# Performance work log

Measured on AMD Instinct MI355X. Metric: run time of the kernel, lower is better.

Reference implementation:

```python
import jax, jax.numpy as jnp
import numpy as np

B, N, D = 8, 1024, 768
H, Z = 12, 64          # num_heads, head_dim (D = H*Z)
HID = 3072             # int(D * mlp_ratio)


def setup_inputs() -> dict:
    key = jax.random.key(0)
    k1, k2, k3, k4 = jax.random.split(key, 4)
    s = 0.02
    x = jax.random.normal(k1, (B, N, D), dtype=jnp.float32)
    Wq = jax.random.normal(k2, (D, D), dtype=jnp.float32) * s
    Wk = jax.random.normal(k3, (D, D), dtype=jnp.float32) * s
    betas = jnp.full((H,), Z ** -0.5, dtype=jnp.float32)
    W_mlp = jax.random.normal(k4, (HID, D), dtype=jnp.float32) * s
    return {"x": x, "Wq": Wq, "Wk": Wk, "betas": betas, "W_mlp": W_mlp}


def reference(x, Wq, Wk, betas, W_mlp):
    # --- KQ-aligned attention ---
    # torch Linear: y = x @ W.T ; weight shape [out=D, in=D]
    Q = jnp.einsum('bnd,ed->bne', x, Wq).reshape(B, N, H, Z).transpose(0, 2, 1, 3)  # bhqz
    K = jnp.einsum('bnd,ed->bne', x, Wk).reshape(B, N, H, Z).transpose(0, 2, 1, 3)  # bhkz
    Wq_r = Wq.reshape(H, Z, D)
    Wk_r = Wk.reshape(H, Z, D)
    F1 = jnp.einsum('hzd,bhkz->bkhd', Wq_r, K)
    F2 = jnp.einsum('hzd,bhqz->bqhd', Wk_r, Q)
    scores = jnp.einsum('bhqz,bhkz,h->bhqk', Q, K, betas)
    attn = jax.nn.softmax(scores, axis=-1)
    T1 = jnp.einsum('bkhd,bhqk->bqd', F1, attn)
    T2 = jnp.einsum('bqhd,bhqk->bkd', F2, attn)
    # --- symmetric-weight Hopfield MLP (bias=False) ---
    hid = jax.nn.relu(jnp.einsum('bnd,hd->bnh', x, W_mlp))
    mlp = jnp.einsum('bnh,hd->bnd', hid, W_mlp)
    return T1 + T2 + mlp
```

## Files before the change

### kernel.cpp

```cpp
#include <hip/hip_runtime.h>
#include <hip/hip_bf16.h>

#define Bq 8
#define Nq 1024
#define Dq 768
#define Hq 12
#define Zq 64
#define HIDq 3072
#define BN (Bq*Nq)
#define QKP 1536

typedef unsigned short u16;
typedef short s16x8 __attribute__((ext_vector_type(8)));
typedef float f32x4 __attribute__((ext_vector_type(4)));
typedef unsigned short u16x4 __attribute__((ext_vector_type(4)));

#define MFMA16 __builtin_amdgcn_mfma_f32_16x16x32_bf16
#define GLOAD16(g, l) __builtin_amdgcn_global_load_lds( \
    (const __attribute__((address_space(1))) void*)(const void*)(g), \
    (__attribute__((address_space(3))) void*)(l), 16, 0, 0)

__device__ __forceinline__ u16 f2bf(float f) {
  unsigned u = __float_as_uint(f);
  return (u16)((u + 0x7FFFu + ((u >> 16) & 1u)) >> 16);
}

__device__ __forceinline__ void xcd_swizzle(int gx, int gy, int& bx, int& by) {
  int l = blockIdx.y * gx + blockIdx.x;
  int c = l & 7, j = l >> 3;
  by = c * (gy >> 3) + j / gx;
  bx = j % gx;
}

__global__ __launch_bounds__(256) void cvt_bf16(const float* __restrict__ in,
                                                u16* __restrict__ out, int n) {
  int i = (blockIdx.x * 256 + threadIdx.x) * 4;
  if (i >= n) return;
  float4 v = *(const float4*)&in[i];
  u16x4 o; o[0] = f2bf(v.x); o[1] = f2bf(v.y); o[2] = f2bf(v.z); o[3] = f2bf(v.w);
  *(u16x4*)&out[i] = o;
}

__global__ __launch_bounds__(256) void cvt_tr(const float* __restrict__ in,
                                              u16* __restrict__ out, u16* __restrict__ outT,
                                              int C, int out_p, int outT_p) {
  __shared__ u16 T[64][72];
  const int t = threadIdx.x;
  const int r0 = blockIdx.y * 64, c0 = blockIdx.x * 64;
  const int r = t >> 3, c8 = (t & 7) * 8;
#pragma unroll
  for (int p = 0; p < 2; p++) {
    const float* ip = &in[(size_t)(r0 + r + p * 32) * C + c0 + c8];
    float4 v0 = *(const float4*)ip, v1 = *(const float4*)(ip + 4);
    u16 tmp[8] = {f2bf(v0.x), f2bf(v0.y), f2bf(v0.z), f2bf(v0.w),
                  f2bf(v1.x), f2bf(v1.y), f2bf(v1.z), f2bf(v1.w)};
    *(uint4*)&out[(size_t)(r0 + r + p * 32) * out_p + c0 + c8] = *(uint4*)tmp;
    *(uint4*)&T[r + p * 32][c8] = *(uint4*)tmp;
  }
  __syncthreads();
#pragma unroll
  for (int p = 0; p < 2; p++) {
    int oc = r + p * 32;
    u16 tmp[8];
#pragma unroll
    for (int j = 0; j < 8; j++) tmp[j] = T[c8 + j][oc];
    *(uint4*)&outT[(size_t)(c0 + oc) * outT_p + r0 + c8] = *(uint4*)tmp;
  }
}

__global__ __launch_bounds__(256) void transpose_bf16(
    const u16* __restrict__ in, u16* __restrict__ out,
    int in_pitch, int out_pitch, int inner_n,
    long in_bs_o, long in_bs_i, long out_bs_o, long out_bs_i) {
  __shared__ u16 T[64][72];
  const int t = threadIdx.x;
  const int bz = blockIdx.z;
  const long iboff = (long)(bz / inner_n) * in_bs_o + (long)(bz % inner_n) * in_bs_i;
  const long oboff = (long)(bz / inner_n) * out_bs_o + (long)(bz % inner_n) * out_bs_i;
  const u16* ip = in + iboff + (long)(blockIdx.y * 64) * in_pitch + blockIdx.x * 64;
  u16* op = out + oboff + (long)(blockIdx.x * 64) * out_pitch + blockIdx.y * 64;
  const int r = t >> 3, c8 = (t & 7) * 8;
#pragma unroll
  for (int p = 0; p < 2; p++)
    *(uint4*)&T[r + p * 32][c8] = *(const uint4*)(ip + (size_t)(r + p * 32) * in_pitch + c8);
  __syncthreads();
#pragma unroll
  for (int p = 0; p < 2; p++) {
    int oc = r + p * 32;
    u16 tmp[8];
#pragma unroll
    for (int j = 0; j < 8; j++) tmp[j] = T[c8 + j][oc];
    *(uint4*)(op + (size_t)oc * out_pitch + c8) = *(uint4*)tmp;
  }
}

template<bool RELU>
__global__ __launch_bounds__(256) void gemm_bf16(
    const u16* __restrict__ A, const u16* __restrict__ B, u16* __restrict__ C,
    int M, int N, int K) {
  __shared__ u16 As[2][128 * 32];
  __shared__ u16 Bs[2][128 * 32];
  int bx, by;
  xcd_swizzle(gridDim.x, gridDim.y, bx, by);
  const int t = threadIdx.x, l = t & 63, w = t >> 6;
  const int lq = l & 15, quad = l >> 4;
  const int bm = by * 128, bn = bx * 128;
  const int wm = (w & 1) * 64, wn = (w >> 1) * 64;
  f32x4 acc[4][4];
#pragma unroll
  for (int i = 0; i < 4; i++)
#pragma unroll
    for (int j = 0; j < 4; j++) acc[i][j] = (f32x4){0.f, 0.f, 0.f, 0.f};

  auto stage = [&](int k0, int bufi) {
#pragma unroll
    for (int p = 0; p < 2; p++) {
      int idx = p * 256 + t;
      GLOAD16(A + (size_t)(bm + (idx >> 2)) * K + k0 + (idx & 3) * 8, &As[bufi][idx * 8]);
      GLOAD16(B + (size_t)(bn + (idx >> 2)) * K + k0 + (idx & 3) * 8, &Bs[bufi][idx * 8]);
    }
  };
  stage(0, 0);
  const int nIter = K >> 5;
  for (int it = 0; it < nIter; it++) {
    __syncthreads();
    if (it + 1 < nIter) stage((it + 1) * 32, (it + 1) & 1);
    const int bi = it & 1;
    s16x8 af[4], bf[4];
#pragma unroll
    for (int mt = 0; mt < 4; mt++)
      af[mt] = *(const s16x8*)&As[bi][(wm + mt * 16 + lq) * 32 + quad * 8];
#pragma unroll
    for (int nt = 0; nt < 4; nt++)
      bf[nt] = *(const s16x8*)&Bs[bi][(wn + nt * 16 + lq) * 32 + quad * 8];
#pragma unroll
    for (int mt = 0; mt < 4; mt++)
#pragma unroll
      for (int nt = 0; nt < 4; nt++)
        acc[mt][nt] = MFMA16(af[mt], bf[nt], acc[mt][nt], 0, 0, 0);
  }
#pragma unroll
  for (int mt = 0; mt < 4; mt++)
#pragma unroll
    for (int nt = 0; nt < 4; nt++) {
      int row = bm + wm + mt * 16 + quad * 4;
      int col = bn + wn + nt * 16 + lq;
#pragma unroll
      for (int r = 0; r < 4; r++) {
        float v = acc[mt][nt][r];
        if (RELU) v = fmaxf(v, 0.f);
        C[(size_t)(row + r) * N + col] = f2bf(v);
      }
    }
}

__global__ __launch_bounds__(256) void gemm_out2(
    const u16* __restrict__ AV12, const u16* __restrict__ hid,
    const u16* __restrict__ WqkT, const u16* __restrict__ WmT,
    float* __restrict__ out) {
  __shared__ u16 As[2][128 * 64];
  __shared__ u16 Bs[2][64 * 64];
  int bx, by;
  xcd_swizzle(gridDim.x, gridDim.y, bx, by);
  const int t = threadIdx.x, l = t & 63, w = t >> 6;
  const int lq = l & 15, quad = l >> 4;
  const int bm = by * 128, bn = bx * 64;
  const int wm = w * 32;
  f32x4 acc[2][4];
#pragma unroll
  for (int i = 0; i < 2; i++)
#pragma unroll
    for (int j = 0; j < 4; j++) acc[i][j] = (f32x4){0.f, 0.f, 0.f, 0.f};

  auto stage = [&](int tl, int bufi) {
    const u16* A; const u16* B; int pitch, k0;
    if (tl < 24) { A = AV12; B = WqkT; pitch = QKP;  k0 = tl * 64; }
    else         { A = hid;  B = WmT;  pitch = HIDq; k0 = (tl - 24) * 64; }
#pragma unroll
    for (int p = 0; p < 4; p++) {
      int idx = p * 256 + t, ks = idx >> 9, rem = idx & 511;
      GLOAD16(A + (size_t)(bm + (rem >> 2)) * pitch + k0 + ks * 32 + (rem & 3) * 8,
              &As[bufi][idx * 8]);
    }
#pragma unroll
    for (int p = 0; p < 2; p++) {
      int idx = p * 256 + t, ks = idx >> 8, rem = idx & 255;
      GLOAD16(B + (size_t)(bn + (rem >> 2)) * pitch + k0 + ks * 32 + (rem & 3) * 8,
              &Bs[bufi][idx * 8]);
    }
  };
  stage(0, 0);
  for (int tl = 0; tl < 72; tl++) {
    __syncthreads();
    if (tl + 1 < 72) stage(tl + 1, (tl + 1) & 1);
    const int bi = tl & 1;
#pragma unroll
    for (int ks = 0; ks < 2; ks++) {
      s16x8 af[2], bf[4];
#pragma unroll
      for (int mt = 0; mt < 2; mt++)
        af[mt] = *(const s16x8*)&As[bi][ks * 4096 + (wm + mt * 16 + lq) * 32 + quad * 8];
#pragma unroll
      for (int nt = 0; nt < 4; nt++)
        bf[nt] = *(const s16x8*)&Bs[bi][ks * 2048 + (nt * 16 + lq) * 32 + quad * 8];
#pragma unroll
      for (int mt = 0; mt < 2; mt++)
#pragma unroll
        for (int nt = 0; nt < 4; nt++)
          acc[mt][nt] = MFMA16(af[mt], bf[nt], acc[mt][nt], 0, 0, 0);
    }
  }
#pragma unroll
  for (int mt = 0; mt < 2; mt++)
#pragma unroll
    for (int nt = 0; nt < 4; nt++) {
      int row = bm + wm + mt * 16 + quad * 4;
      int col = bn + nt * 16 + lq;
#pragma unroll
      for (int r = 0; r < 4; r++)
        out[(size_t)(row + r) * Dq + col] = acc[mt][nt][r];
    }
}

__global__ __launch_bounds__(256) void attn_pass1(
    const u16* __restrict__ QKb, const u16* __restrict__ KbT,
    const float* __restrict__ betas, u16* __restrict__ AV12,
    float* __restrict__ lg) {
  __shared__ u16 Qs[2][64][32];
  __shared__ u16 Ks[2][64][32];
  __shared__ u16 Kts[2][64][32];
  __shared__ u16 Ps[64][72];
  __shared__ float red[4][64];
  __shared__ float li[64];

  const int t = threadIdx.x, l = t & 63, w = t >> 6;
  const int lq = l & 15, quad = l >> 4;
  const int c = blockIdx.x & 7, j = blockIdx.x >> 3;
  const int bh = c * 12 + j / 16, qt = j % 16;
  const int b = bh / Hq, h = bh % Hq;
  const int q0 = qt * 64;
  const float beta = betas[h];
  const u16* Qh = QKb + (size_t)(b * Nq) * QKP + h * 64;
  const u16* Kh = Qh + Dq;
  const u16* KTh = KbT + (size_t)bh * 64 * Nq;
  u16* QsF = &Qs[0][0][0]; u16* KsF = &Ks[0][0][0]; u16* KtsF = &Kts[0][0][0];

#pragma unroll
  for (int p = 0; p < 2; p++) {
    int idx = p * 256 + t;
    GLOAD16(Qh + (size_t)(q0 + ((idx >> 2) & 63)) * QKP + (idx >> 8) * 32 + (idx & 3) * 8,
            QsF + idx * 8);
  }
  __syncthreads();
  s16x8 bqf[2][4];
#pragma unroll
  for (int zs = 0; zs < 2; zs++)
#pragma unroll
    for (int nt = 0; nt < 4; nt++)
      bqf[zs][nt] = *(const s16x8*)&Qs[zs][nt * 16 + lq][quad * 8];

  float lsum[4] = {0.f, 0.f, 0.f, 0.f};
  f32x4 ao[4];
#pragma unroll
  for (int nt = 0; nt < 4; nt++) ao[nt] = (f32x4){0.f, 0.f, 0.f, 0.f};

  for (int kt = 0; kt < 16; kt++) {
#pragma unroll
    for (int p = 0; p < 2; p++) {
      int idx = p * 256 + t;
      GLOAD16(Kh + (size_t)(kt * 64 + ((idx >> 2) & 63)) * QKP + (idx >> 8) * 32 + (idx & 3) * 8,
              KsF + idx * 8);
      GLOAD16(KTh + (size_t)((idx >> 2) & 63) * Nq + kt * 64 + (idx >> 8) * 32 + (idx & 3) * 8,
              KtsF + idx * 8);
    }
    __syncthreads();
    f32x4 sc[4];
#pragma unroll
    for (int nt = 0; nt < 4; nt++) sc[nt] = (f32x4){0.f, 0.f, 0.f, 0.f};
#pragma unroll
    for (int zs = 0; zs < 2; zs++) {
      s16x8 a = *(const s16x8*)&Ks[zs][w * 16 + lq][quad * 8];
#pragma unroll
      for (int nt = 0; nt < 4; nt++)
        sc[nt] = MFMA16(a, bqf[zs][nt], sc[nt], 0, 0, 0);
    }
#pragma unroll
    for (int nt = 0; nt < 4; nt++) {
      u16x4 pk;
#pragma unroll
      for (int r = 0; r < 4; r++) {
        float e = __expf(sc[nt][r] * beta);
        lsum[nt] += e;
        pk[r] = f2bf(e);
      }
      *(u16x4*)&Ps[nt * 16 + lq][w * 16 + quad * 4] = pk;
    }
    __syncthreads();
#pragma unroll
    for (int ks = 0; ks < 2; ks++) {
      s16x8 a = *(const s16x8*)&Ps[w * 16 + lq][ks * 32 + quad * 8];
#pragma unroll
      for (int nt = 0; nt < 4; nt++) {
        s16x8 bk = *(const s16x8*)&Kts[ks][nt * 16 + lq][quad * 8];
        ao[nt] = MFMA16(a, bk, ao[nt], 0, 0, 0);
      }
    }
    __syncthreads();
  }
#pragma unroll
  for (int nt = 0; nt < 4; nt++) {
    float v = lsum[nt];
    v += __shfl_xor(v, 16, 64);
    v += __shfl_xor(v, 32, 64);
    if (l < 16) red[w][nt * 16 + lq] = v;
  }
  __syncthreads();
  if (t < 64) {
    float s = red[0][t] + red[1][t] + red[2][t] + red[3][t];
    lg[(size_t)bh * Nq + q0 + t] = s;
    li[t] = 1.0f / s;
  }
  __syncthreads();
  u16* Oh = AV12 + (size_t)(b * Nq + q0) * QKP + h * 64;
  float lr[4];
#pragma unroll
  for (int r = 0; r < 4; r++) lr[r] = li[w * 16 + quad * 4 + r];
#pragma unroll
  for (int nt = 0; nt < 4; nt++)
#pragma unroll
    for (int r = 0; r < 4; r++)
      Oh[(size_t)(w * 16 + quad * 4 + r) * QKP + nt * 16 + lq] = f2bf(ao[nt][r] * lr[r]);
}

__global__ __launch_bounds__(256) void attn_pass2(
    const u16* __restrict__ QKb, const u16* __restrict__ QbT,
    const float* __restrict__ betas, u16* __restrict__ AV12,
    const float* __restrict__ lg) {
  __shared__ u16 Qs[2][64][32];
  __shared__ u16 Qts[2][64][32];
  __shared__ u16 Ks[2][64][32];
  __shared__ u16 Pts[64][72];
  __shared__ float li_s[64];

  const int t = threadIdx.x, l = t & 63, w = t >> 6;
  const int lq = l & 15, quad = l >> 4;
  const int c = blockIdx.x & 7, j = blockIdx.x >> 3;
  const int bh = c * 12 + j / 16, kt = j % 16;
  const int b = bh / Hq, h = bh % Hq;
  const int k0 = kt * 64;
  const float beta = betas[h];
  const u16* Qh = QKb + (size_t)(b * Nq) * QKP + h * 64;
  const u16* Kh = Qh + Dq;
  const u16* QTh = QbT + (size_t)bh * 64 * Nq;
  u16* QsF = &Qs[0][0][0]; u16* QtsF = &Qts[0][0][0]; u16* KsF = &Ks[0][0][0];

#pragma unroll
  for (int p = 0; p < 2; p++) {
    int idx = p * 256 + t;
    GLOAD16(Kh + (size_t)(k0 + ((idx >> 2) & 63)) * QKP + (idx >> 8) * 32 + (idx & 3) * 8,
            KsF + idx * 8);
  }
  __syncthreads();
  s16x8 bkf[2][4];
#pragma unroll
  for (int zs = 0; zs < 2; zs++)
#pragma unroll
    for (int nt = 0; nt < 4; nt++)
      bkf[zs][nt] = *(const s16x8*)&Ks[zs][nt * 16 + lq][quad * 8];

  f32x4 ao[4];
#pragma unroll
  for (int nt = 0; nt < 4; nt++) ao[nt] = (f32x4){0.f, 0.f, 0.f, 0.f};

  for (int qt = 0; qt < 16; qt++) {
#pragma unroll
    for (int p = 0; p < 2; p++) {
      int idx = p * 256 + t;
      GLOAD16(Qh + (size_t)(qt * 64 + ((idx >> 2) & 63)) * QKP + (idx >> 8) * 32 + (idx & 3) * 8,
              QsF + idx * 8);
      GLOAD16(QTh + (size_t)((idx >> 2) & 63) * Nq + qt * 64 + (idx >> 8) * 32 + (idx & 3) * 8,
              QtsF + idx * 8);
    }
    if (t < 64) li_s[t] = 1.0f / lg[(size_t)bh * Nq + qt * 64 + t];
    __syncthreads();
    f32x4 sc[4];
#pragma unroll
    for (int nt = 0; nt < 4; nt++) sc[nt] = (f32x4){0.f, 0.f, 0.f, 0.f};
#pragma unroll
    for (int zs = 0; zs < 2; zs++) {
      s16x8 a = *(const s16x8*)&Qs[zs][w * 16 + lq][quad * 8];
#pragma unroll
      for (int nt = 0; nt < 4; nt++)
        sc[nt] = MFMA16(a, bkf[zs][nt], sc[nt], 0, 0, 0);
    }
    float lr[4];
#pragma unroll
    for (int r = 0; r < 4; r++) lr[r] = li_s[w * 16 + quad * 4 + r];
#pragma unroll
    for (int nt = 0; nt < 4; nt++) {
      u16x4 pk;
#pragma unroll
      for (int r = 0; r < 4; r++)
        pk[r] = f2bf(__expf(sc[nt][r] * beta) * lr[r]);
      *(u16x4*)&Pts[nt * 16 + lq][w * 16 + quad * 4] = pk;
    }
    __syncthreads();
#pragma unroll
    for (int qs = 0; qs < 2; qs++) {
      s16x8 a = *(const s16x8*)&Pts[w * 16 + lq][qs * 32 + quad * 8];
#pragma unroll
      for (int nt = 0; nt < 4; nt++) {
        s16x8 bq = *(const s16x8*)&Qts[qs][nt * 16 + lq][quad * 8];
        ao[nt] = MFMA16(a, bq, ao[nt], 0, 0, 0);
      }
    }
    __syncthreads();
  }
  u16* Oh = AV12 + (size_t)(b * Nq + k0) * QKP + Dq + h * 64;
#pragma unroll
  for (int nt = 0; nt < 4; nt++)
#pragma unroll
    for (int r = 0; r < 4; r++)
      Oh[(size_t)(w * 16 + quad * 4 + r) * QKP + nt * 16 + lq] = f2bf(ao[nt][r]);
}

extern "C" void kernel_launch(void* const* d_in, const int* in_sizes, int n_in,
                              void* d_out, int out_size, void* d_ws, size_t ws_size,
                              hipStream_t stream) {
  const float* x     = (const float*)d_in[0];
  const float* Wq    = (const float*)d_in[1];
  const float* Wk    = (const float*)d_in[2];
  const float* betas = (const float*)d_in[3];
  const float* Wm    = (const float*)d_in[4];
  float* out = (float*)d_out;

  u16* xb   = (u16*)d_ws;
  u16* Wqkb = xb + (size_t)BN * Dq;
  u16* Wmb  = Wqkb + (size_t)QKP * Dq;
  u16* WqkT = Wmb + (size_t)HIDq * Dq;
  u16* QKb  = WqkT + (size_t)Dq * QKP;
  u16* QbT  = QKb + (size_t)BN * QKP;
  u16* KbT  = QbT + (size_t)Bq * Hq * Zq * Nq;
  u16* AV12 = KbT + (size_t)Bq * Hq * Zq * Nq;
  float* lg = (float*)(AV12 + (size_t)BN * QKP);
  u16* hidb = QKb;
  u16* WmT  = xb;

  dim3 blk(256);
  cvt_bf16<<<(BN * Dq) / 1024, blk, 0, stream>>>(x, xb, BN * Dq);
  cvt_tr<<<dim3(12, 12), blk, 0, stream>>>(Wq, Wqkb, WqkT, Dq, Dq, QKP);
  cvt_tr<<<dim3(12, 12), blk, 0, stream>>>(Wk, Wqkb + (size_t)Dq * Dq, WqkT + Dq, Dq, Dq, QKP);
  cvt_bf16<<<(HIDq * Dq) / 1024, blk, 0, stream>>>(Wm, Wmb, HIDq * Dq);

  gemm_bf16<false><<<dim3(QKP / 128, BN / 128), blk, 0, stream>>>(
      xb, Wqkb, QKb, BN, QKP, Dq);

  transpose_bf16<<<dim3(1, 16, 96), blk, 0, stream>>>(QKb, QbT, QKP, Nq, Hq,
      (long)Nq * QKP, 64, (long)Hq * 64 * Nq, (long)64 * Nq);
  transpose_bf16<<<dim3(1, 16, 96), blk, 0, stream>>>(QKb + Dq, KbT, QKP, Nq, Hq,
      (long)Nq * QKP, 64, (long)Hq * 64 * Nq, (long)64 * Nq);

  attn_pass1<<<Bq * Hq * 16, blk, 0, stream>>>(QKb, KbT, betas, AV12, lg);
  attn_pass2<<<Bq * Hq * 16, blk, 0, stream>>>(QKb, QbT, betas, AV12, lg);

  gemm_bf16<true><<<dim3(HIDq / 128, BN / 128), blk, 0, stream>>>(
      xb, Wmb, hidb, BN, HIDq, Dq);

  transpose_bf16<<<dim3(12, 48, 1), blk, 0, stream>>>(Wmb, WmT, Dq, HIDq, 1, 0, 0, 0, 0);

  gemm_out2<<<dim3(Dq / 64, BN / 128), blk, 0, stream>>>(AV12, hidb, WqkT, WmT, out);
}
```

Before: 363.8 us.

## Split-K final output GEMM across three z-slices with atomic accumulation

The final output GEMM (attention AV12×WqkT plus hidden×WmT, K=4608) is split along K into three 1536-wide slices, one per grid z-index. Each block now computes a larger 128×128 tile with a 32-wide k-step, and partial results are combined with float atomic adds into an output that is zeroed by a memset first. The aim is to put more blocks in flight (the original grid had only 768 blocks each running a long 72-step K loop) and to reuse each staged tile across more MFMAs. The cost is atomic traffic on the fp32 output, an extra memset pass, and a summation order that is no longer deterministic.

```diff
diff --git a/kernel.cpp b/kernel.cpp
--- a/kernel.cpp
+++ b/kernel.cpp
@@ -158,67 +158,62 @@
     const u16* __restrict__ AV12, const u16* __restrict__ hid,
     const u16* __restrict__ WqkT, const u16* __restrict__ WmT,
     float* __restrict__ out) {
-  __shared__ u16 As[2][128 * 64];
-  __shared__ u16 Bs[2][64 * 64];
+  __shared__ u16 As[2][128 * 32];
+  __shared__ u16 Bs[2][128 * 32];
   int bx, by;
   xcd_swizzle(gridDim.x, gridDim.y, bx, by);
+  const int z = blockIdx.z;
   const int t = threadIdx.x, l = t & 63, w = t >> 6;
   const int lq = l & 15, quad = l >> 4;
-  const int bm = by * 128, bn = bx * 64;
-  const int wm = w * 32;
-  f32x4 acc[2][4];
-#pragma unroll
-  for (int i = 0; i < 2; i++)
+  const int bm = by * 128, bn = bx * 128;
+  const int wm = (w & 1) * 64, wn = (w >> 1) * 64;
+
+  const u16* A; const u16* B; int pitch, kbase;
+  if (z == 0) { A = AV12; B = WqkT; pitch = QKP;  kbase = 0; }
+  else        { A = hid;  B = WmT;  pitch = HIDq; kbase = (z - 1) * 1536; }
+
+  f32x4 acc[4][4];
+#pragma unroll
+  for (int i = 0; i < 4; i++)
 #pragma unroll
     for (int j = 0; j < 4; j++) acc[i][j] = (f32x4){0.f, 0.f, 0.f, 0.f};
 
   auto stage = [&](int tl, int bufi) {
-    const u16* A; const u16* B; int pitch, k0;
-    if (tl < 24) { A = AV12; B = WqkT; pitch = QKP;  k0 = tl * 64; }
-    else         { A = hid;  B = WmT;  pitch = HIDq; k0 = (tl - 24) * 64; }
-#pragma unroll
-    for (int p = 0; p < 4; p++) {
-      int idx = p * 256 + t, ks = idx >> 9, rem = idx & 511;
-      GLOAD16(A + (size_t)(bm + (rem >> 2)) * pitch + k0 + ks * 32 + (rem & 3) * 8,
-              &As[bufi][idx * 8]);
-    }
+    const int k0 = kbase + tl * 32;
 #pragma unroll
     for (int p = 0; p < 2; p++) {
-      int idx = p * 256 + t, ks = idx >> 8, rem = idx & 255;
-      GLOAD16(B + (size_t)(bn + (rem >> 2)) * pitch + k0 + ks * 32 + (rem & 3) * 8,
-              &Bs[bufi][idx * 8]);
+      int idx = p * 256 + t;
+      GLOAD16(A + (size_t)(bm + (idx >> 2)) * pitch + k0 + (idx & 3) * 8, &As[bufi][idx * 8]);
+      GLOAD16(B + (size_t)(bn + (idx >> 2)) * pitch + k0 + (idx & 3) * 8, &Bs[bufi][idx * 8]);
     }
   };
   stage(0, 0);
-  for (int tl = 0; tl < 72; tl++) {
-    __syncthreads();
-    if (tl + 1 < 72) stage(tl + 1, (tl + 1) & 1);
+  for (int tl = 0; tl < 48; tl++) {
+    __syncthreads();
+    if (tl + 1 < 48) stage(tl + 1, (tl + 1) & 1);
     const int bi = tl & 1;
-#pragma unroll
-    for (int ks = 0; ks < 2; ks++) {
-      s16x8 af[2], bf[4];
-#pragma unroll
-      for (int mt = 0; mt < 2; mt++)
-        af[mt] = *(const s16x8*)&As[bi][ks * 4096 + (wm + mt * 16 + lq) * 32 + quad * 8];
+    s16x8 af[4], bf[4];
+#pragma unroll
+    for (int mt = 0; mt < 4; mt++)
+      af[mt] = *(const s16x8*)&As[bi][(wm + mt * 16 + lq) * 32 + quad * 8];
+#pragma unroll
+    for (int nt = 0; nt < 4; nt++)
+      bf[nt] = *(const s16x8*)&Bs[bi][(wn + nt * 16 + lq) * 32 + quad * 8];
+#pragma unroll
+    for (int mt = 0; mt < 4; mt++)
 #pragma unroll
       for (int nt = 0; nt < 4; nt++)
-        bf[nt] = *(const s16x8*)&Bs[bi][ks * 2048 + (nt * 16 + lq) * 32 + quad * 8];
-#pragma unroll
-      for (int mt = 0; mt < 2; mt++)
-#pragma unroll
-        for (int nt = 0; nt < 4; nt++)
-          acc[mt][nt] = MFMA16(af[mt], bf[nt], acc[mt][nt], 0, 0, 0);
-    }
-  }
-#pragma unroll
-  for (int mt = 0; mt < 2; mt++)
+        acc[mt][nt] = MFMA16(af[mt], bf[nt], acc[mt][nt], 0, 0, 0);
+  }
+#pragma unroll
+  for (int mt = 0; mt < 4; mt++)
 #pragma unroll
     for (int nt = 0; nt < 4; nt++) {
       int row = bm + wm + mt * 16 + quad * 4;
-      int col = bn + nt * 16 + lq;
+      int col = bn + wn + nt * 16 + lq;
 #pragma unroll
       for (int r = 0; r < 4; r++)
-        out[(size_t)(row + r) * Dq + col] = acc[mt][nt][r];
+        unsafeAtomicAdd(&out[(size_t)(row + r) * Dq + col], acc[mt][nt][r]);
     }
 }
 
@@ -447,6 +442,9 @@
   u16* WmT  = xb;
 
   dim3 blk(256);
+
+  hipMemsetAsync(out, 0, (size_t)BN * Dq * sizeof(float), stream);
+
   cvt_bf16<<<(BN * Dq) / 1024, blk, 0, stream>>>(x, xb, BN * Dq);
   cvt_tr<<<dim3(12, 12), blk, 0, stream>>>(Wq, Wqkb, WqkT, Dq, Dq, QKP);
   cvt_tr<<<dim3(12, 12), blk, 0, stream>>>(Wk, Wqkb + (size_t)Dq * Dq, WqkT + Dq, Dq, Dq, QKP);
@@ -468,5 +466,5 @@
 
   transpose_bf16<<<dim3(12, 48, 1), blk, 0, stream>>>(Wmb, WmT, Dq, HIDq, 1, 0, 0, 0, 0);
 
-  gemm_out2<<<dim3(Dq / 64, BN / 128), blk, 0, stream>>>(AV12, hidb, WqkT, WmT, out);
-}
+  gemm_out2<<<dim3(Dq / 128, BN / 128, 3), blk, 0, stream>>>(AV12, hidb, WqkT, WmT, out);
+}
```

After: 420.9 us. 15.7% more time.

## Double-buffer K/Q tile staging in both attention passes

Applied to the files above, without the earlier changes.

Both attention kernels now keep two LDS buffers for the streamed K/K^T (pass 1) and Q/Q^T/inverse-sum (pass 2) tiles. The next tile's global-to-LDS load is issued at the top of each iteration, before the current tile's MFMA work. The trailing barrier is removed, leaving one barrier per iteration plus the existing mid-loop barrier. The aim is to hide global load latency behind compute, at the cost of roughly doubling the staging LDS. The mid-loop barrier may force the prefetch to complete early and limit the overlap.

```diff
diff --git a/kernel.cpp b/kernel.cpp
--- a/kernel.cpp
+++ b/kernel.cpp
@@ -227,8 +227,8 @@
     const float* __restrict__ betas, u16* __restrict__ AV12,
     float* __restrict__ lg) {
   __shared__ u16 Qs[2][64][32];
-  __shared__ u16 Ks[2][64][32];
-  __shared__ u16 Kts[2][64][32];
+  __shared__ u16 Ks[2][2][64][32];
+  __shared__ u16 Kts[2][2][64][32];
   __shared__ u16 Ps[64][72];
   __shared__ float red[4][64];
   __shared__ float li[64];
@@ -243,7 +243,7 @@
   const u16* Qh = QKb + (size_t)(b * Nq) * QKP + h * 64;
   const u16* Kh = Qh + Dq;
   const u16* KTh = KbT + (size_t)bh * 64 * Nq;
-  u16* QsF = &Qs[0][0][0]; u16* KsF = &Ks[0][0][0]; u16* KtsF = &Kts[0][0][0];
+  u16* QsF = &Qs[0][0][0];
 
 #pragma unroll
   for (int p = 0; p < 2; p++) {
@@ -251,35 +251,41 @@
     GLOAD16(Qh + (size_t)(q0 + ((idx >> 2) & 63)) * QKP + (idx >> 8) * 32 + (idx & 3) * 8,
             QsF + idx * 8);
   }
-  __syncthreads();
-  s16x8 bqf[2][4];
-#pragma unroll
-  for (int zs = 0; zs < 2; zs++)
-#pragma unroll
-    for (int nt = 0; nt < 4; nt++)
-      bqf[zs][nt] = *(const s16x8*)&Qs[zs][nt * 16 + lq][quad * 8];
-
-  float lsum[4] = {0.f, 0.f, 0.f, 0.f};
-  f32x4 ao[4];
-#pragma unroll
-  for (int nt = 0; nt < 4; nt++) ao[nt] = (f32x4){0.f, 0.f, 0.f, 0.f};
-
-  for (int kt = 0; kt < 16; kt++) {
+
+  auto stageK = [&](int kt, int bufi) {
 #pragma unroll
     for (int p = 0; p < 2; p++) {
       int idx = p * 256 + t;
       GLOAD16(Kh + (size_t)(kt * 64 + ((idx >> 2) & 63)) * QKP + (idx >> 8) * 32 + (idx & 3) * 8,
-              KsF + idx * 8);
+              &Ks[bufi][0][0][0] + idx * 8);
       GLOAD16(KTh + (size_t)((idx >> 2) & 63) * Nq + kt * 64 + (idx >> 8) * 32 + (idx & 3) * 8,
-              KtsF + idx * 8);
-    }
-    __syncthreads();
+              &Kts[bufi][0][0][0] + idx * 8);
+    }
+  };
+  stageK(0, 0);
+  __syncthreads();
+  s16x8 bqf[2][4];
+#pragma unroll
+  for (int zs = 0; zs < 2; zs++)
+#pragma unroll
+    for (int nt = 0; nt < 4; nt++)
+      bqf[zs][nt] = *(const s16x8*)&Qs[zs][nt * 16 + lq][quad * 8];
+
+  float lsum[4] = {0.f, 0.f, 0.f, 0.f};
+  f32x4 ao[4];
+#pragma unroll
+  for (int nt = 0; nt < 4; nt++) ao[nt] = (f32x4){0.f, 0.f, 0.f, 0.f};
+
+  for (int kt = 0; kt < 16; kt++) {
+    if (kt) __syncthreads();
+    if (kt + 1 < 16) stageK(kt + 1, (kt + 1) & 1);
+    const int bi = kt & 1;
     f32x4 sc[4];
 #pragma unroll
     for (int nt = 0; nt < 4; nt++) sc[nt] = (f32x4){0.f, 0.f, 0.f, 0.f};
 #pragma unroll
     for (int zs = 0; zs < 2; zs++) {
-      s16x8 a = *(const s16x8*)&Ks[zs][w * 16 + lq][quad * 8];
+      s16x8 a = *(const s16x8*)&Ks[bi][zs][w * 16 + lq][quad * 8];
 #pragma unroll
       for (int nt = 0; nt < 4; nt++)
         sc[nt] = MFMA16(a, bqf[zs][nt], sc[nt], 0, 0, 0);
@@ -301,11 +307,10 @@
       s16x8 a = *(const s16x8*)&Ps[w * 16 + lq][ks * 32 + quad * 8];
 #pragma unroll
       for (int nt = 0; nt < 4; nt++) {
-        s16x8 bk = *(const s16x8*)&Kts[ks][nt * 16 + lq][quad * 8];
+        s16x8 bk = *(const s16x8*)&Kts[bi][ks][nt * 16 + lq][quad * 8];
         ao[nt] = MFMA16(a, bk, ao[nt], 0, 0, 0);
       }
     }
-    __syncthreads();
   }
 #pragma unroll
   for (int nt = 0; nt < 4; nt++) {
@@ -336,11 +341,11 @@
     const u16* __restrict__ QKb, const u16* __restrict__ QbT,
     const float* __restrict__ betas, u16* __restrict__ AV12,
     const float* __restrict__ lg) {
-  __shared__ u16 Qs[2][64][32];
-  __shared__ u16 Qts[2][64][32];
   __shared__ u16 Ks[2][64][32];
+  __shared__ u16 Qs[2][2][64][32];
+  __shared__ u16 Qts[2][2][64][32];
   __shared__ u16 Pts[64][72];
-  __shared__ float li_s[64];
+  __shared__ float li_s[2][64];
 
   const int t = threadIdx.x, l = t & 63, w = t >> 6;
   const int lq = l & 15, quad = l >> 4;
@@ -352,7 +357,7 @@
   const u16* Qh = QKb + (size_t)(b * Nq) * QKP + h * 64;
   const u16* Kh = Qh + Dq;
   const u16* QTh = QbT + (size_t)bh * 64 * Nq;
-  u16* QsF = &Qs[0][0][0]; u16* QtsF = &Qts[0][0][0]; u16* KsF = &Ks[0][0][0];
+  u16* KsF = &Ks[0][0][0];
 
 #pragma unroll
   for (int p = 0; p < 2; p++) {
@@ -360,42 +365,48 @@
     GLOAD16(Kh + (size_t)(k0 + ((idx >> 2) & 63)) * QKP + (idx >> 8) * 32 + (idx & 3) * 8,
             KsF + idx * 8);
   }
-  __syncthreads();
-  s16x8 bkf[2][4];
-#pragma unroll
-  for (int zs = 0; zs < 2; zs++)
-#pragma unroll
-    for (int nt = 0; nt < 4; nt++)
-      bkf[zs][nt] = *(const s16x8*)&Ks[zs][nt * 16 + lq][quad * 8];
-
-  f32x4 ao[4];
-#pragma unroll
-  for (int nt = 0; nt < 4; nt++) ao[nt] = (f32x4){0.f, 0.f, 0.f, 0.f};
-
-  for (int qt = 0; qt < 16; qt++) {
+
+  auto stageQ = [&](int qt, int bufi) {
 #pragma unroll
     for (int p = 0; p < 2; p++) {
       int idx = p * 256 + t;
       GLOAD16(Qh + (size_t)(qt * 64 + ((idx >> 2) & 63)) * QKP + (idx >> 8) * 32 + (idx & 3) * 8,
-              QsF + idx * 8);
+              &Qs[bufi][0][0][0] + idx * 8);
       GLOAD16(QTh + (size_t)((idx >> 2) & 63) * Nq + qt * 64 + (idx >> 8) * 32 + (idx & 3) * 8,
-              QtsF + idx * 8);
-    }
-    if (t < 64) li_s[t] = 1.0f / lg[(size_t)bh * Nq + qt * 64 + t];
-    __syncthreads();
+              &Qts[bufi][0][0][0] + idx * 8);
+    }
+    if (t < 64) li_s[bufi][t] = 1.0f / lg[(size_t)bh * Nq + qt * 64 + t];
+  };
+  stageQ(0, 0);
+  __syncthreads();
+  s16x8 bkf[2][4];
+#pragma unroll
+  for (int zs = 0; zs < 2; zs++)
+#pragma unroll
+    for (int nt = 0; nt < 4; nt++)
+      bkf[zs][nt] = *(const s16x8*)&Ks[zs][nt * 16 + lq][quad * 8];
+
+  f32x4 ao[4];
+#pragma unroll
+  for (int nt = 0; nt < 4; nt++) ao[nt] = (f32x4){0.f, 0.f, 0.f, 0.f};
+
+  for (int qt = 0; qt < 16; qt++) {
+    if (qt) __syncthreads();
+    if (qt + 1 < 16) stageQ(qt + 1, (qt + 1) & 1);
+    const int bi = qt & 1;
     f32x4 sc[4];
 #pragma unroll
     for (int nt = 0; nt < 4; nt++) sc[nt] = (f32x4){0.f, 0.f, 0.f, 0.f};
 #pragma unroll
     for (int zs = 0; zs < 2; zs++) {
-      s16x8 a = *(const s16x8*)&Qs[zs][w * 16 + lq][quad * 8];
+      s16x8 a = *(const s16x8*)&Qs[bi][zs][w * 16 + lq][quad * 8];
 #pragma unroll
       for (int nt = 0; nt < 4; nt++)
         sc[nt] = MFMA16(a, bkf[zs][nt], sc[nt], 0, 0, 0);
     }
     float lr[4];
 #pragma unroll
-    for (int r = 0; r < 4; r++) lr[r] = li_s[w * 16 + quad * 4 + r];
+    for (int r = 0; r < 4; r++) lr[r] = li_s[bi][w * 16 + quad * 4 + r];
 #pragma unroll
     for (int nt = 0; nt < 4; nt++) {
       u16x4 pk;
@@ -410,11 +421,10 @@
       s16x8 a = *(const s16x8*)&Pts[w * 16 + lq][qs * 32 + quad * 8];
 #pragma unroll
       for (int nt = 0; nt < 4; nt++) {
-        s16x8 bq = *(const s16x8*)&Qts[qs][nt * 16 + lq][quad * 8];
+        s16x8 bq = *(const s16x8*)&Qts[bi][qs][nt * 16 + lq][quad * 8];
         ao[nt] = MFMA16(a, bq, ao[nt], 0, 0, 0);
       }
     }
-    __syncthreads();
   }
   u16* Oh = AV12 + (size_t)(b * Nq + k0) * QKP + Dq + h * 64;
 #pragma unroll
```

Measured after the change: 372.4 us. 2.4% more time.
